# Performance work log

Measured on AMD Instinct MI355X. Metric: run time of the kernel, lower is better.

Reference implementation:

```python
import jax, jax.numpy as jnp
import numpy as np

EPS = 1e-12  # F.normalize eps

def _l2norm(x):
    n = jnp.linalg.norm(x, axis=-1, keepdims=True)
    return x / jnp.maximum(n, EPS)

def setup_inputs() -> dict:
    key = jax.random.key(0)
    ks = jax.random.split(key, 12)
    B, C, D, N, K = 64, 256, 128, 100000, 8
    inp = {
        "query_input": jax.random.normal(ks[0], (B, C), dtype=jnp.float32),
        "keys": jax.random.normal(ks[1], (N, D), dtype=jnp.float32),
        "values": jax.random.normal(ks[2], (N, D), dtype=jnp.float32),
        "importance": jax.random.uniform(ks[3], (N,), dtype=jnp.float32),
        # params (Linear weights stored torch-style: [out, in])
        "W_q": jax.random.normal(ks[4], (D, C), dtype=jnp.float32) / np.sqrt(C),
        "b_q": jax.random.normal(ks[5], (D,), dtype=jnp.float32) * 0.01,
        "w_attn": jax.random.normal(ks[6], (D,), dtype=jnp.float32) / np.sqrt(D),
        "b_attn": jax.random.normal(ks[7], (), dtype=jnp.float32) * 0.01,
        "W_comb": jax.random.normal(ks[8], (D, D), dtype=jnp.float32) / np.sqrt(D),
        "b_comb": jax.random.normal(ks[9], (D,), dtype=jnp.float32) * 0.01,
        "top_k": K,
    }
    return inp

def reference(query_input, keys, values, importance, W_q, b_q, w_attn, b_attn, W_comb, b_comb, top_k):
    # query projection: [B, D]
    q = query_input @ W_q.T + b_q
    # cosine similarity against every bank entry, importance-weighted: [B, N]
    sim = (_l2norm(q) @ _l2norm(keys).T) * importance[None, :]
    # top-k entries per batch row
    _, idx = jax.lax.top_k(sim, top_k)          # [B, K]
    retrieved = values[idx]                      # [B, K, D] gather
    # attention over the K retrieved memories
    scores = jax.nn.softmax(retrieved @ w_attn + b_attn, axis=-1)  # [B, K]
    memory_output = jnp.einsum("bk,bkd->bd", scores, retrieved)
    return memory_output @ W_comb.T + b_comb
```

## Files before the change

### kernel.cpp

```cpp
#include <hip/hip_runtime.h>

typedef __attribute__((ext_vector_type(8))) short short8;
typedef __attribute__((ext_vector_type(4))) float f32x4;

#define BB 64
#define CC 256
#define DD 128
#define NN 100000
#define KK 8

#define CHUNK 128
#define NBLK ((NN + CHUNK - 1) / CHUNK)
#define CPB (NBLK * KK)

__device__ __forceinline__ unsigned short f2bf(float x) {
    unsigned u = __float_as_uint(x);
    unsigned r = u + 0x7fffu + ((u >> 16) & 1u);
    return (unsigned short)(r >> 16);
}

__device__ __forceinline__ void split_bf(float x, unsigned short& h, unsigned short& l) {
    h = f2bf(x);
    float hf = __uint_as_float(((unsigned)h) << 16);
    l = f2bf(x - hf);
}

__device__ __forceinline__ void bfins8(float x, float l[8]) {
#pragma unroll
    for (int s = 0; s < 8; ++s) {
        float hi = fmaxf(l[s], x);
        x = fminf(l[s], x);
        l[s] = hi;
    }
}

__device__ __forceinline__ void bpins8(float v, int ix, float lv[8], int li[8]) {
#pragma unroll
    for (int s = 0; s < 8; ++s) {
        const bool gt = v > lv[s];
        const float nv = gt ? lv[s] : v;
        const int   ni = gt ? li[s] : ix;
        lv[s] = gt ? v : lv[s];
        li[s] = gt ? ix : li[s];
        v = nv; ix = ni;
    }
}

__device__ __forceinline__ void merge8(const float a[8], const float b[8], float o[8]) {
    float m[8];
#pragma unroll
    for (int i = 0; i < 8; ++i) m[i] = fmaxf(a[i], b[7 - i]);
#define CE(i, j) { float hi = fmaxf(m[i], m[j]); float lo = fminf(m[i], m[j]); m[i] = hi; m[j] = lo; }
    CE(0, 4) CE(1, 5) CE(2, 6) CE(3, 7)
    CE(0, 2) CE(1, 3) CE(4, 6) CE(5, 7)
    CE(0, 1) CE(2, 3) CE(4, 5) CE(6, 7)
#undef CE
#pragma unroll
    for (int i = 0; i < 8; ++i) o[i] = m[i];
}

__global__ __launch_bounds__(128) void qproj_kernel(
    const float* __restrict__ query,
    const float* __restrict__ Wq,
    const float* __restrict__ bq,
    unsigned short* __restrict__ qAhi,
    unsigned short* __restrict__ qAlo)
{
    __shared__ float qrow[CC];
    const int tid = threadIdx.x;
    const int b = blockIdx.x;
    for (int i = tid; i < CC; i += 128) qrow[i] = query[b * CC + i];
    __syncthreads();
    float acc = bq[tid];
    const float4* wr = reinterpret_cast<const float4*>(Wq + (size_t)tid * CC);
#pragma unroll 8
    for (int c = 0; c < CC / 4; ++c) {
        float4 w = wr[c];
        acc = fmaf(w.x, qrow[c * 4 + 0], acc);
        acc = fmaf(w.y, qrow[c * 4 + 1], acc);
        acc = fmaf(w.z, qrow[c * 4 + 2], acc);
        acc = fmaf(w.w, qrow[c * 4 + 3], acc);
    }
    unsigned short h, l;
    split_bf(acc, h, l);
    const int d = tid;
    const int mt = b >> 4, n = b & 15;
    const int ks = d >> 5, quad = (d >> 3) & 3, j = d & 7;
    const size_t fi = ((size_t)(mt * 4 + ks) * 64 + quad * 16 + n) * 8 + j;
    qAhi[fi] = h;
    qAlo[fi] = l;
}

__global__ __launch_bounds__(256, 5) void simtopk_kernel(
    const unsigned short* __restrict__ qAhi,
    const unsigned short* __restrict__ qAlo,
    const float* __restrict__ keys,
    const float* __restrict__ imp,
    float* __restrict__ cand_v)
{
    __shared__ float sims[64 * 128];

    const int tid = threadIdx.x;
    const int w = tid >> 6, lane = tid & 63;
    const int p = w >> 1;
    const int h = w & 1;
    const int blk = blockIdx.x;
    const int key0 = blk * CHUNK;
    const int n = lane & 15, quad = lane >> 4;

    short8 Ah[2][4], Al[2][4];
    {
        const short8* GH = reinterpret_cast<const short8*>(qAhi);
        const short8* GL = reinterpret_cast<const short8*>(qAlo);
#pragma unroll
        for (int m2 = 0; m2 < 2; ++m2)
#pragma unroll
            for (int ks = 0; ks < 4; ++ks) {
                const int idx = ((p * 2 + m2) * 4 + ks) * 64 + lane;
                Ah[m2][ks] = GH[idx];
                Al[m2][ks] = GL[idx];
            }
    }

#pragma unroll
    for (int t = 0; t < 4; ++t) {
        const int jl = h * 64 + t * 16 + n;
        const int j = key0 + jl;
        const int jc = (j < NN) ? j : (NN - 1);
        const float* kb = keys + (size_t)jc * DD + quad * 8;

        f32x4 acc[2];
        acc[0] = (f32x4){0.f, 0.f, 0.f, 0.f};
        acc[1] = (f32x4){0.f, 0.f, 0.f, 0.f};
        float ss = 0.f;

#pragma unroll
        for (int ks = 0; ks < 4; ++ks) {
            const float4 b0 = *reinterpret_cast<const float4*>(kb + ks * 32);
            const float4 b1 = *reinterpret_cast<const float4*>(kb + ks * 32 + 4);
            const float f[8] = {b0.x, b0.y, b0.z, b0.w, b1.x, b1.y, b1.z, b1.w};
            unsigned hw[4], lw[4];
#pragma unroll
            for (int e = 0; e < 4; ++e) {
                const float f0 = f[2 * e], f1 = f[2 * e + 1];
                const unsigned u0 = __float_as_uint(f0), u1 = __float_as_uint(f1);
                hw[e] = __builtin_amdgcn_perm(u1, u0, 0x07060302u);
                const float d0 = f0 - __uint_as_float(u0 & 0xffff0000u);
                const float d1 = f1 - __uint_as_float(u1 & 0xffff0000u);
                lw[e] = __builtin_amdgcn_perm(__float_as_uint(d1), __float_as_uint(d0), 0x07060302u);
                ss = fmaf(f0, f0, fmaf(f1, f1, ss));
            }
            uint4 hv = {hw[0], hw[1], hw[2], hw[3]};
            uint4 lv = {lw[0], lw[1], lw[2], lw[3]};
            short8 Bh = *reinterpret_cast<short8*>(&hv);
            short8 Bl = *reinterpret_cast<short8*>(&lv);
#pragma unroll
            for (int m2 = 0; m2 < 2; ++m2) {
                acc[m2] = __builtin_amdgcn_mfma_f32_16x16x32_bf16(Ah[m2][ks], Bh, acc[m2], 0, 0, 0);
                acc[m2] = __builtin_amdgcn_mfma_f32_16x16x32_bf16(Ah[m2][ks], Bl, acc[m2], 0, 0, 0);
                acc[m2] = __builtin_amdgcn_mfma_f32_16x16x32_bf16(Al[m2][ks], Bh, acc[m2], 0, 0, 0);
            }
        }

        ss += __shfl_xor(ss, 16);
        ss += __shfl_xor(ss, 32);
        const bool valid = (j < NN);
        float scale = 0.f;
        if (valid) scale = imp[j] / fmaxf(sqrtf(ss), 1e-12f);

#pragma unroll
        for (int m2 = 0; m2 < 2; ++m2)
#pragma unroll
            for (int r = 0; r < 4; ++r) {
                const int row = (p * 2 + m2) * 16 + quad * 4 + r;
                const float v = valid ? acc[m2][r] * scale : -1e30f;
                const unsigned packed = (__float_as_uint(v) & ~0x7Fu) | (unsigned)jl;
                sims[row * 128 + (jl ^ ((row & 4) << 2))] = __uint_as_float(packed);
            }
    }
    __syncthreads();

    float v8[8];
    {
        const int row = tid >> 2, part = tid & 3;
#pragma unroll
        for (int s = 0; s < 8; ++s) v8[s] = -1e30f;
        const float* rp = &sims[row * 128 + part * 32];
        const int sc = (row & 15) ^ (part << 3);
        for (int i = 0; i < 32; ++i)
            bfins8(rp[(i ^ sc) & 31], v8);
    }
    __syncthreads();

    {
        const int row = tid >> 2, part = tid & 3;
        const int rot = (row & 7) * 4;
#pragma unroll
        for (int s = 0; s < 8; ++s)
            sims[row * 128 + ((4 * s + part + rot) & 31)] = v8[s];
    }
    __syncthreads();

    if (tid < 64) {
        const int row = tid;
        const int rot = (row & 7) * 4;
        float l0[8], l1[8], l2[8], l3[8];
#pragma unroll
        for (int s = 0; s < 8; ++s) {
            const float* rp = &sims[row * 128];
            l0[s] = rp[(4 * s + 0 + rot) & 31];
            l1[s] = rp[(4 * s + 1 + rot) & 31];
            l2[s] = rp[(4 * s + 2 + rot) & 31];
            l3[s] = rp[(4 * s + 3 + rot) & 31];
        }
        float m01[8], m23[8], m8[8];
        merge8(l0, l1, m01);
        merge8(l2, l3, m23);
        merge8(m01, m23, m8);
        float4* out4 = reinterpret_cast<float4*>(cand_v + (size_t)row * CPB + (size_t)blk * KK);
        out4[0] = (float4){m8[0], m8[1], m8[2], m8[3]};
        out4[1] = (float4){m8[4], m8[5], m8[6], m8[7]};
    }
}

__global__ __launch_bounds__(256) void mergefinish_kernel(
    const float* __restrict__ cand_v,
    const float* __restrict__ values,
    const float* __restrict__ w_attn,
    const float* __restrict__ b_attn,
    const float* __restrict__ W_comb,
    const float* __restrict__ b_comb,
    float* __restrict__ out)
{
    __shared__ float lv[256 * 8];
    __shared__ int   li[256 * 8];
    __shared__ int   tk[KK];
    __shared__ float red[KK][DD];
    __shared__ float tvals[KK];
    __shared__ float mem[DD];

    const int tid = threadIdx.x;
    const int row = blockIdx.x;

    {
        float v8[8]; int i8[8];
#pragma unroll
        for (int s = 0; s < 8; ++s) { v8[s] = -1e30f; i8[s] = 0; }
        const float4* cv4 = reinterpret_cast<const float4*>(cand_v + (size_t)row * CPB);
        for (int c4 = tid; c4 < CPB / 4; c4 += 256) {
            const float4 v = cv4[c4];
            const int c = c4 * 4;
            bpins8(v.x, c + 0, v8, i8);
            bpins8(v.y, c + 1, v8, i8);
            bpins8(v.z, c + 2, v8, i8);
            bpins8(v.w, c + 3, v8, i8);
        }
#pragma unroll
        for (int s = 0; s < 8; ++s) { lv[tid * 8 + s] = v8[s]; li[tid * 8 + s] = i8[s]; }
    }
    __syncthreads();

    if (tid < 64) {
        float m8[8]; int mi8[8];
#pragma unroll
        for (int s = 0; s < 8; ++s) { m8[s] = -1e30f; mi8[s] = 0; }
        for (int k2 = 0; k2 < 4; ++k2)
#pragma unroll
            for (int s = 0; s < 8; ++s)
                bpins8(lv[(tid + 64 * k2) * 8 + s], li[(tid + 64 * k2) * 8 + s], m8, mi8);
        for (int rd = 0; rd < KK; ++rd) {
            float m = m8[0];
#pragma unroll
            for (int d = 1; d < 64; d <<= 1) m = fmaxf(m, __shfl_xor(m, d));
            const unsigned long long msk = __ballot(m8[0] == m);
            const int wl = (int)(__ffsll((long long)msk) - 1);
            const int wc = __shfl(mi8[0], wl);
            if (tid == 0)
                tk[rd] = (wc >> 3) * CHUNK + (int)(__float_as_uint(m) & 127u);
            if (tid == wl) {
#pragma unroll
                for (int s = 0; s < 7; ++s) { m8[s] = m8[s + 1]; mi8[s] = mi8[s + 1]; }
                m8[7] = -1e30f;
            }
        }
    }
    __syncthreads();

    float vk[KK];
    if (tid < 128) {
#pragma unroll
        for (int k = 0; k < KK; ++k)
            vk[k] = values[(size_t)tk[k] * DD + tid];
        const float wa = w_attn[tid];
#pragma unroll
        for (int k = 0; k < KK; ++k) red[k][tid] = vk[k] * wa;
    }
    __syncthreads();
    if (tid < KK) {
        float s = 0.f;
        for (int i = 0; i < DD; ++i) s += red[tid][i];
        tvals[tid] = s + b_attn[0];
    }
    __syncthreads();
    if (tid < 128) {
        float m = tvals[0];
#pragma unroll
        for (int k = 1; k < KK; ++k) m = fmaxf(m, tvals[k]);
        float e[KK]; float se = 0.f;
#pragma unroll
        for (int k = 0; k < KK; ++k) { e[k] = expf(tvals[k] - m); se += e[k]; }
        const float inv = 1.f / se;
        float md = 0.f;
#pragma unroll
        for (int k = 0; k < KK; ++k) md += (e[k] * inv) * vk[k];
        mem[tid] = md;
    }
    __syncthreads();
    if (tid < 128) {
        float acc = b_comb[tid];
        const float4* wrow = reinterpret_cast<const float4*>(W_comb + (size_t)tid * DD);
#pragma unroll 8
        for (int c = 0; c < DD / 4; ++c) {
            float4 wv = wrow[c];
            acc = fmaf(wv.x, mem[c * 4 + 0], acc);
            acc = fmaf(wv.y, mem[c * 4 + 1], acc);
            acc = fmaf(wv.z, mem[c * 4 + 2], acc);
            acc = fmaf(wv.w, mem[c * 4 + 3], acc);
        }
        out[row * DD + tid] = acc;
    }
}

extern "C" void kernel_launch(void* const* d_in, const int* in_sizes, int n_in,
                              void* d_out, int out_size, void* d_ws, size_t ws_size,
                              hipStream_t stream) {
    const float* query  = (const float*)d_in[0];
    const float* keys   = (const float*)d_in[1];
    const float* values = (const float*)d_in[2];
    const float* imp    = (const float*)d_in[3];
    const float* Wq     = (const float*)d_in[4];
    const float* bq     = (const float*)d_in[5];
    const float* wattn  = (const float*)d_in[6];
    const float* battn  = (const float*)d_in[7];
    const float* Wcomb  = (const float*)d_in[8];
    const float* bcomb  = (const float*)d_in[9];

    unsigned short* qAhi = (unsigned short*)d_ws;
    unsigned short* qAlo = qAhi + 8192;
    float* cand_v = (float*)(qAlo + 8192);

    qproj_kernel<<<BB, 128, 0, stream>>>(query, Wq, bq, qAhi, qAlo);
    simtopk_kernel<<<NBLK, 256, 0, stream>>>(qAhi, qAlo, keys, imp, cand_v);
    mergefinish_kernel<<<BB, 256, 0, stream>>>(cand_v, values, wattn, battn,
                                               Wcomb, bcomb, (float*)d_out);
}
```

Before: 172.8 us.

## Replace serial insertion top-8 with sorting-network merges and padded LDS rows

Each thread's top-8 selection over 32 candidates now uses two sort8 networks plus bitonic merges instead of 32 serial 8-deep insertions. This shortens the dependency chain and cuts the compare count. The shared sims rows are padded to 132 floats in place of the XOR swizzle, and all key loads for a tile are issued up front before the conversions. Occupancy hint drops from 5 to 4 waves per SIMD to leave room for the extra registers, at the risk of less latency hiding.

```diff
diff --git a/kernel.cpp b/kernel.cpp
--- a/kernel.cpp
+++ b/kernel.cpp
@@ -23,15 +23,6 @@
     h = f2bf(x);
     float hf = __uint_as_float(((unsigned)h) << 16);
     l = f2bf(x - hf);
-}
-
-__device__ __forceinline__ void bfins8(float x, float l[8]) {
-#pragma unroll
-    for (int s = 0; s < 8; ++s) {
-        float hi = fmaxf(l[s], x);
-        x = fminf(l[s], x);
-        l[s] = hi;
-    }
 }
 
 __device__ __forceinline__ void bpins8(float v, int ix, float lv[8], int li[8]) {
@@ -46,18 +37,28 @@
     }
 }
 
+#define CE(i, j) { float hi = fmaxf(m[i], m[j]); float lo = fminf(m[i], m[j]); m[i] = hi; m[j] = lo; }
+
+__device__ __forceinline__ void sort8(float m[8]) {
+    CE(0, 1) CE(2, 3) CE(4, 5) CE(6, 7)
+    CE(0, 2) CE(1, 3) CE(4, 6) CE(5, 7)
+    CE(1, 2) CE(5, 6)
+    CE(0, 4) CE(1, 5) CE(2, 6) CE(3, 7)
+    CE(2, 4) CE(3, 5)
+    CE(1, 2) CE(3, 4) CE(5, 6)
+}
+
 __device__ __forceinline__ void merge8(const float a[8], const float b[8], float o[8]) {
     float m[8];
 #pragma unroll
     for (int i = 0; i < 8; ++i) m[i] = fmaxf(a[i], b[7 - i]);
-#define CE(i, j) { float hi = fmaxf(m[i], m[j]); float lo = fminf(m[i], m[j]); m[i] = hi; m[j] = lo; }
     CE(0, 4) CE(1, 5) CE(2, 6) CE(3, 7)
     CE(0, 2) CE(1, 3) CE(4, 6) CE(5, 7)
     CE(0, 1) CE(2, 3) CE(4, 5) CE(6, 7)
+#pragma unroll
+    for (int i = 0; i < 8; ++i) o[i] = m[i];
+}
 #undef CE
-#pragma unroll
-    for (int i = 0; i < 8; ++i) o[i] = m[i];
-}
 
 __global__ __launch_bounds__(128) void qproj_kernel(
     const float* __restrict__ query,
@@ -91,14 +92,14 @@
     qAlo[fi] = l;
 }
 
-__global__ __launch_bounds__(256, 5) void simtopk_kernel(
+__global__ __launch_bounds__(256, 4) void simtopk_kernel(
     const unsigned short* __restrict__ qAhi,
     const unsigned short* __restrict__ qAlo,
     const float* __restrict__ keys,
     const float* __restrict__ imp,
     float* __restrict__ cand_v)
 {
-    __shared__ float sims[64 * 128];
+    __shared__ float sims[64 * 132];
 
     const int tid = threadIdx.x;
     const int w = tid >> 6, lane = tid & 63;
@@ -129,6 +130,13 @@
         const int jc = (j < NN) ? j : (NN - 1);
         const float* kb = keys + (size_t)jc * DD + quad * 8;
 
+        float4 bv[8];
+#pragma unroll
+        for (int ks = 0; ks < 4; ++ks) {
+            bv[2 * ks]     = *reinterpret_cast<const float4*>(kb + ks * 32);
+            bv[2 * ks + 1] = *reinterpret_cast<const float4*>(kb + ks * 32 + 4);
+        }
+
         f32x4 acc[2];
         acc[0] = (f32x4){0.f, 0.f, 0.f, 0.f};
         acc[1] = (f32x4){0.f, 0.f, 0.f, 0.f};
@@ -136,9 +144,8 @@
 
 #pragma unroll
         for (int ks = 0; ks < 4; ++ks) {
-            const float4 b0 = *reinterpret_cast<const float4*>(kb + ks * 32);
-            const float4 b1 = *reinterpret_cast<const float4*>(kb + ks * 32 + 4);
-            const float f[8] = {b0.x, b0.y, b0.z, b0.w, b1.x, b1.y, b1.z, b1.w};
+            const float f[8] = {bv[2*ks].x, bv[2*ks].y, bv[2*ks].z, bv[2*ks].w,
+                                bv[2*ks+1].x, bv[2*ks+1].y, bv[2*ks+1].z, bv[2*ks+1].w};
             unsigned hw[4], lw[4];
 #pragma unroll
             for (int e = 0; e < 4; ++e) {
@@ -175,7 +182,7 @@
                 const int row = (p * 2 + m2) * 16 + quad * 4 + r;
                 const float v = valid ? acc[m2][r] * scale : -1e30f;
                 const unsigned packed = (__float_as_uint(v) & ~0x7Fu) | (unsigned)jl;
-                sims[row * 128 + (jl ^ ((row & 4) << 2))] = __uint_as_float(packed);
+                sims[row * 132 + jl] = __uint_as_float(packed);
             }
     }
     __syncthreads();
@@ -183,35 +190,45 @@
     float v8[8];
     {
         const int row = tid >> 2, part = tid & 3;
-#pragma unroll
-        for (int s = 0; s < 8; ++s) v8[s] = -1e30f;
-        const float* rp = &sims[row * 128 + part * 32];
-        const int sc = (row & 15) ^ (part << 3);
-        for (int i = 0; i < 32; ++i)
-            bfins8(rp[(i ^ sc) & 31], v8);
+        const float* rp = &sims[row * 132 + part * 32];
+        const int st = ((row & 15) + part * 8) & 31;
+        float a[8], b[8], c8[8], d8[8];
+#pragma unroll
+        for (int s = 0; s < 8; ++s) {
+            a[s] = rp[(s + st) & 31];
+            b[s] = rp[(s + 8 + st) & 31];
+        }
+        sort8(a); sort8(b);
+        merge8(a, b, c8);
+#pragma unroll
+        for (int s = 0; s < 8; ++s) {
+            a[s] = rp[(s + 16 + st) & 31];
+            b[s] = rp[(s + 24 + st) & 31];
+        }
+        sort8(a); sort8(b);
+        merge8(a, b, d8);
+        merge8(c8, d8, v8);
     }
     __syncthreads();
 
     {
         const int row = tid >> 2, part = tid & 3;
-        const int rot = (row & 7) * 4;
 #pragma unroll
         for (int s = 0; s < 8; ++s)
-            sims[row * 128 + ((4 * s + part + rot) & 31)] = v8[s];
+            sims[row * 132 + ((part * 8 + s + row) & 31)] = v8[s];
     }
     __syncthreads();
 
     if (tid < 64) {
         const int row = tid;
-        const int rot = (row & 7) * 4;
+        const float* rp = &sims[row * 132];
         float l0[8], l1[8], l2[8], l3[8];
 #pragma unroll
         for (int s = 0; s < 8; ++s) {
-            const float* rp = &sims[row * 128];
-            l0[s] = rp[(4 * s + 0 + rot) & 31];
-            l1[s] = rp[(4 * s + 1 + rot) & 31];
-            l2[s] = rp[(4 * s + 2 + rot) & 31];
-            l3[s] = rp[(4 * s + 3 + rot) & 31];
+            l0[s] = rp[(s + row) & 31];
+            l1[s] = rp[(8 + s + row) & 31];
+            l2[s] = rp[(16 + s + row) & 31];
+            l3[s] = rp[(24 + s + row) & 31];
         }
         float m01[8], m23[8], m8[8];
         merge8(l0, l1, m01);
```

Result: faster. 163.0 us (-5.7%).
